# Performance work log

Measured on AMD Instinct MI355X. Metric: run time of the kernel, lower is better.

## Reference

```python
import jax, jax.numpy as jnp
import numpy as np
import math

WINDOW = 1024
B, H, E, D = 4, 8, 64, 64


def setup_inputs() -> dict:
    key = jax.random.key(0)
    kq, kk, kv, ks = jax.random.split(key, 4)
    queries = jax.random.normal(kq, (B, WINDOW, H, E), dtype=jnp.float32)
    keys = jax.random.normal(kk, (B, WINDOW, H, E), dtype=jnp.float32)
    values = jax.random.normal(kv, (B, WINDOW, H, D), dtype=jnp.float32)
    sigma = jax.random.normal(ks, (B, WINDOW, H), dtype=jnp.float32)
    return {"queries": queries, "keys": keys, "values": values, "sigma": sigma}


def reference(queries, keys, values, sigma):
    # queries: [B,L,H,E], keys: [B,S,H,E], values: [B,S,H,D], sigma: [B,L,H]
    Bq, L, Hh, Ee = queries.shape
    scale = 1.0 / math.sqrt(Ee)
    # scores: [B,H,L,S]
    attn = scale * jnp.einsum('blhe,bshe->bhls', queries, keys)
    win = attn.shape[-1]

    # sigma path: [B,L,H] -> [B,H,L]
    sig = jnp.transpose(sigma, (0, 2, 1))
    sig = jax.nn.sigmoid(sig * 5.0) + 1e-5
    sig = jnp.power(3.0, sig) - 1.0          # [B,H,L]
    sig = jnp.broadcast_to(sig[..., None], sig.shape + (win,))  # [B,H,L,S]

    # |i-j| distance matrix [L,S]
    idx = jnp.arange(win, dtype=jnp.float32)
    dist = jnp.abs(idx[:, None] - idx[None, :])

    inv_sqrt_2pi = 1.0 / math.sqrt(2.0 * math.pi)
    prior = inv_sqrt_2pi / sig * jnp.exp(-(dist ** 2) / 2.0 / (sig ** 2))

    series = jax.nn.softmax(attn, axis=-1)   # [B,H,L,S]
    V = jnp.einsum('bhls,bshd->blhd', series, values)
    return V, series, prior, sig
```

## Files before the change

kernel.cpp:

```cpp
#include <hip/hip_runtime.h>
#include <math.h>


typedef __attribute__((ext_vector_type(8))) short short8;
typedef __attribute__((ext_vector_type(4))) float f32x4;

constexpr int Bc = 4, Lc = 1024, Hc = 8, Ec = 64, Dc = 64, Sc = 1024;

constexpr long OFF_V      = 0;
constexpr long OFF_SERIES = (long)Bc * Lc * Hc * Dc;
constexpr long OFF_PRIOR  = OFF_SERIES + (long)Bc * Hc * Lc * Sc;
constexpr long OFF_SIG    = OFF_PRIOR  + (long)Bc * Hc * Lc * Sc;

constexpr long KELEMS = (long)Bc * Lc * Hc * Ec;

#define LOG2E        1.4426950408889634f
#define LOG2_3       1.5849625007211562f
#define INV_SQRT_2PI 0.3989422804014327f
#define HALF_LOG2E   0.7213475204444817f
#define FIVE_LOG2E   7.213475204444817f

__device__ __forceinline__ unsigned short f2bf(float x) {
    unsigned int u = __float_as_uint(x);
    return (unsigned short)((u + 0x7fffu + ((u >> 16) & 1u)) >> 16);
}
__device__ __forceinline__ float bf2f(unsigned short h) {
    return __uint_as_float(((unsigned int)h) << 16);
}
__device__ __forceinline__ void split8(const float* v, short8& hi, short8& lo) {
    #pragma unroll
    for (int j = 0; j < 8; ++j) {
        unsigned short hh = f2bf(v[j]);
        hi[j] = (short)hh;
        lo[j] = (short)f2bf(v[j] - bf2f(hh));
    }
}

__global__ __launch_bounds__(256)
void k_prep(const float* __restrict__ kp, unsigned short* __restrict__ khi,
            unsigned short* __restrict__ klo)
{
    const int i = blockIdx.x * 256 + threadIdx.x;
    const int e4 = i & 15, h = (i >> 4) & 7, s = (i >> 7) & 1023, b = i >> 17;
    const float4 v = reinterpret_cast<const float4*>(kp)[((b * Lc + s) * Hc + h) * 16 + e4];
    const unsigned short h0 = f2bf(v.x), h1 = f2bf(v.y), h2 = f2bf(v.z), h3 = f2bf(v.w);
    uint2 hi, lo;
    hi.x = (unsigned)h0 | ((unsigned)h1 << 16);
    hi.y = (unsigned)h2 | ((unsigned)h3 << 16);
    lo.x = (unsigned)f2bf(v.x - bf2f(h0)) | ((unsigned)f2bf(v.y - bf2f(h1)) << 16);
    lo.y = (unsigned)f2bf(v.z - bf2f(h2)) | ((unsigned)f2bf(v.w - bf2f(h3)) << 16);
    const long dst = ((long)(b * Hc + h) * Lc + s) * 16 + e4;
    reinterpret_cast<uint2*>(khi)[dst] = hi;
    reinterpret_cast<uint2*>(klo)[dst] = lo;
}

__global__ __launch_bounds__(256)
void v_prep(const float* __restrict__ vp, unsigned short* __restrict__ vthi,
            unsigned short* __restrict__ vtlo)
{
    __shared__ float lds[64][68];
    const int blk = blockIdx.x;
    const int bh = blk >> 4, s0 = (blk & 15) * 64;
    const int b = bh >> 3, h = bh & 7;
    const int t = threadIdx.x;
    {
        const int sl = t >> 4, d4 = t & 15;
        #pragma unroll
        for (int r = 0; r < 4; ++r) {
            const int s = sl + r * 16;
            const float4 v = reinterpret_cast<const float4*>(
                vp)[((long)(b * Lc + s0 + s) * Hc + h) * 16 + d4];
            *reinterpret_cast<float4*>(&lds[s][d4 * 4]) = v;
        }
    }
    __syncthreads();
    const int d = t >> 2, a = t & 3;
    #pragma unroll
    for (int jj = 0; jj < 4; ++jj) {
        const int sb = a * 16 + jj * 4;
        const float x0 = lds[sb + 0][d], x1 = lds[sb + 1][d];
        const float x2 = lds[sb + 2][d], x3 = lds[sb + 3][d];
        const unsigned short h0 = f2bf(x0), h1 = f2bf(x1), h2 = f2bf(x2), h3 = f2bf(x3);
        uint2 hi, lo;
        hi.x = (unsigned)h0 | ((unsigned)h1 << 16);
        hi.y = (unsigned)h2 | ((unsigned)h3 << 16);
        lo.x = (unsigned)f2bf(x0 - bf2f(h0)) | ((unsigned)f2bf(x1 - bf2f(h1)) << 16);
        lo.y = (unsigned)f2bf(x2 - bf2f(h2)) | ((unsigned)f2bf(x3 - bf2f(h3)) << 16);
        const long dst = (((long)bh * Dc + d) * Sc + s0 + sb) >> 2;
        reinterpret_cast<uint2*>(vthi)[dst] = hi;
        reinterpret_cast<uint2*>(vtlo)[dst] = lo;
    }
}

__global__ __launch_bounds__(256, 2)
void attn_all(const float* __restrict__ qp,
              const unsigned short* __restrict__ khi,
              const unsigned short* __restrict__ klo,
              const unsigned short* __restrict__ vthi,
              const unsigned short* __restrict__ vtlo,
              const float* __restrict__ sigp, float* __restrict__ out)
{
    __shared__ float Plds[4][4096];

    const int bid = blockIdx.x;
    const int swz = (bid & 7) * 256 + (bid >> 3);
    const int rowblk = swz & 63, bh = swz >> 6;
    const int b = bh >> 3, h = bh & 7;
    const int row0 = rowblk * 16;
    const int t = threadIdx.x;
    const int w = t >> 6;
    const int lane = t & 63;
    const int ln = lane & 15, kg = lane >> 4;
    float* const Pw = Plds[w];

    short8 qhi[2], qlo[2];
    {
        const float* qrow = qp + ((long)(b * Lc + row0 + ln) * Hc + h) * Ec;
        #pragma unroll
        for (int kc = 0; kc < 2; ++kc) {
            const float* qq = qrow + kc * 32 + kg * 8;
            const float4 qa = *reinterpret_cast<const float4*>(qq);
            const float4 qb = *reinterpret_cast<const float4*>(qq + 4);
            float qv[8] = {qa.x, qa.y, qa.z, qa.w, qb.x, qb.y, qb.z, qb.w};
            split8(qv, qhi[kc], qlo[kc]);
        }
    }

    f32x4 p[16];
    const long kcb = (long)bh * Lc;
    #pragma unroll
    for (int tt = 0; tt < 16; ++tt) {
        const int col = w * 256 + tt * 16 + ln;
        const unsigned short* kb = khi + (kcb + col) * Ec + kg * 8;
        const unsigned short* kl = klo + (kcb + col) * Ec + kg * 8;
        const short8 bh0 = *reinterpret_cast<const short8*>(kb);
        const short8 bl0 = *reinterpret_cast<const short8*>(kl);
        const short8 bh1 = *reinterpret_cast<const short8*>(kb + 32);
        const short8 bl1 = *reinterpret_cast<const short8*>(kl + 32);
        f32x4 a = {0.f, 0.f, 0.f, 0.f};
        a = __builtin_amdgcn_mfma_f32_16x16x32_bf16(qhi[0], bh0, a, 0, 0, 0);
        a = __builtin_amdgcn_mfma_f32_16x16x32_bf16(qlo[0], bh0, a, 0, 0, 0);
        a = __builtin_amdgcn_mfma_f32_16x16x32_bf16(qhi[0], bl0, a, 0, 0, 0);
        a = __builtin_amdgcn_mfma_f32_16x16x32_bf16(qhi[1], bh1, a, 0, 0, 0);
        a = __builtin_amdgcn_mfma_f32_16x16x32_bf16(qlo[1], bh1, a, 0, 0, 0);
        a = __builtin_amdgcn_mfma_f32_16x16x32_bf16(qhi[1], bl1, a, 0, 0, 0);
        p[tt] = a;
    }

    const float C = 0.125f * LOG2E;
    float sl4[4] = {0.f, 0.f, 0.f, 0.f};
    #pragma unroll
    for (int tt = 0; tt < 16; ++tt) {
        #pragma unroll
        for (int i = 0; i < 4; ++i) {
            const float e = __builtin_exp2f(p[tt][i] * C);
            p[tt][i] = e; sl4[i] += e;
        }
    }
    #pragma unroll
    for (int off = 1; off < 16; off <<= 1) {
        #pragma unroll
        for (int i = 0; i < 4; ++i) sl4[i] += __shfl_xor(sl4[i], off, 64);
    }
    if (ln == 0) {
        #pragma unroll
        for (int i = 0; i < 4; ++i) Pw[kg * 4 + i] = sl4[i];
    }
    __syncthreads();
    float inv[4];
    #pragma unroll
    for (int i = 0; i < 4; ++i) {
        const int rr = kg * 4 + i;
        inv[i] = 1.0f / (Plds[0][rr] + Plds[1][rr] + Plds[2][rr] + Plds[3][rr]);
    }
    __syncthreads();

    #pragma unroll
    for (int tt = 0; tt < 16; ++tt) {
        #pragma unroll
        for (int i = 0; i < 4; ++i) {
            const float v = p[tt][i] * inv[i];
            Pw[(kg * 4 + i) * 256 + tt * 16 + ln] = v;
        }
    }

    {
        const long sbase = OFF_SERIES + ((long)bh * Lc + row0) * Sc + w * 256;
        #pragma unroll
        for (int r = 0; r < 16; ++r) {
            const float4 v = *reinterpret_cast<const float4*>(&Pw[r * 256 + lane * 4]);
            *reinterpret_cast<float4*>(&out[sbase + (long)r * Sc + lane * 4]) = v;
        }
    }

    f32x4 acc2[4];
    #pragma unroll
    for (int dt = 0; dt < 4; ++dt) acc2[dt] = (f32x4){0.f, 0.f, 0.f, 0.f};
    #pragma unroll
    for (int kc = 0; kc < 8; ++kc) {
        const float* pa = &Pw[ln * 256 + kc * 32 + kg * 8];
        const float4 a0 = *reinterpret_cast<const float4*>(pa);
        const float4 a1 = *reinterpret_cast<const float4*>(pa + 4);
        float av[8] = {a0.x, a0.y, a0.z, a0.w, a1.x, a1.y, a1.z, a1.w};
        short8 phi, plo;
        split8(av, phi, plo);
        #pragma unroll
        for (int dt = 0; dt < 4; ++dt) {
            const long vb = ((long)bh * Dc + dt * 16 + ln) * Sc + w * 256 + kc * 32 + kg * 8;
            const short8 vh = *reinterpret_cast<const short8*>(vthi + vb);
            const short8 vl = *reinterpret_cast<const short8*>(vtlo + vb);
            acc2[dt] = __builtin_amdgcn_mfma_f32_16x16x32_bf16(phi, vh, acc2[dt], 0, 0, 0);
            acc2[dt] = __builtin_amdgcn_mfma_f32_16x16x32_bf16(plo, vh, acc2[dt], 0, 0, 0);
            acc2[dt] = __builtin_amdgcn_mfma_f32_16x16x32_bf16(phi, vl, acc2[dt], 0, 0, 0);
        }
    }

    #pragma unroll
    for (int dt = 0; dt < 4; ++dt) {
        #pragma unroll
        for (int i = 0; i < 4; ++i)
            Pw[(kg * 4 + i) * 68 + dt * 16 + ln] = acc2[dt][i];
    }
    __syncthreads();
    {
        const int r = t >> 4, d0 = (t & 15) * 4;
        const float4 s0 = *reinterpret_cast<const float4*>(&Plds[0][r * 68 + d0]);
        const float4 s1 = *reinterpret_cast<const float4*>(&Plds[1][r * 68 + d0]);
        const float4 s2 = *reinterpret_cast<const float4*>(&Plds[2][r * 68 + d0]);
        const float4 s3 = *reinterpret_cast<const float4*>(&Plds[3][r * 68 + d0]);
        float4 vs;
        vs.x = s0.x + s1.x + s2.x + s3.x;
        vs.y = s0.y + s1.y + s2.y + s3.y;
        vs.z = s0.z + s1.z + s2.z + s3.z;
        vs.w = s0.w + s1.w + s2.w + s3.w;
        *reinterpret_cast<float4*>(
            &out[OFF_V + ((long)(b * Lc + row0 + r) * Hc + h) * Dc + d0]) = vs;
    }

    {
        const int c0 = t * 4;
        #pragma unroll 4
        for (int r = 0; r < 16; ++r) {
            const int lg = row0 + r;
            const float x = sigp[(long)(b * Lc + lg) * Hc + h];
            const float sgm = 1.0f / (1.0f + __builtin_exp2f(-FIVE_LOG2E * x)) + 1e-5f;
            const float sg = __builtin_exp2f(LOG2_3 * sgm) - 1.0f;
            const float amp = INV_SQRT_2PI / sg;
            const float ce = -HALF_LOG2E / (sg * sg);
            const long rowbase = ((long)bh * Lc + lg) * Sc;
            const float df = (float)(c0 - lg);
            float4 pr;
            pr.x = amp * __builtin_exp2f(ce * df * df);
            const float d1 = df + 1.f; pr.y = amp * __builtin_exp2f(ce * d1 * d1);
            const float d2 = df + 2.f; pr.z = amp * __builtin_exp2f(ce * d2 * d2);
            const float d3 = df + 3.f; pr.w = amp * __builtin_exp2f(ce * d3 * d3);
            *reinterpret_cast<float4*>(&out[OFF_PRIOR + rowbase + c0]) = pr;
            *reinterpret_cast<float4*>(&out[OFF_SIG + rowbase + c0]) =
                make_float4(sg, sg, sg, sg);
        }
    }
}

extern "C" void kernel_launch(void* const* d_in, const int* in_sizes, int n_in,
                              void* d_out, int out_size, void* d_ws, size_t ws_size,
                              hipStream_t stream) {
    const float* q  = (const float*)d_in[0];
    const float* k  = (const float*)d_in[1];
    const float* v  = (const float*)d_in[2];
    const float* sg = (const float*)d_in[3];
    float* out = (float*)d_out;

    unsigned short* khi  = (unsigned short*)d_ws;
    unsigned short* klo  = khi + KELEMS;
    unsigned short* vthi = klo + KELEMS;
    unsigned short* vtlo = vthi + KELEMS;

    hipLaunchKernelGGL(k_prep, dim3(2048), dim3(256), 0, stream, k, khi, klo);
    hipLaunchKernelGGL(v_prep, dim3(512), dim3(256), 0, stream, v, vthi, vtlo);
    hipLaunchKernelGGL(attn_all, dim3(2048), dim3(256), 0, stream,
                       q, khi, klo, vthi, vtlo, sg, out);
}
```

Baseline: 571.3 us.

## Fuse exp into QK loop, defer softmax normalization, and pad LDS rows

Computes exp right after each QK MFMA tile and writes the unnormalized probabilities straight to LDS instead of holding all 16 score tiles in registers. Normalization moves to the series store and the final PV accumulator, which removes one barrier and a separate rescale pass. LDS rows are padded to a pitch of 258 to cut bank conflicts, and the PV loop is reordered so each output tile's accumulation runs to completion. The occupancy hint on launch bounds is dropped. The odd pitch leaves some float4 LDS accesses only 8-byte aligned, which may make them slower or split them.

Result: faster. 553.1 us (-3.2%).

```diff
diff --git a/kernel.cpp b/kernel.cpp
--- a/kernel.cpp
+++ b/kernel.cpp
@@ -19,6 +19,8 @@
 #define INV_SQRT_2PI 0.3989422804014327f
 #define HALF_LOG2E   0.7213475204444817f
 #define FIVE_LOG2E   7.213475204444817f
+
+#define PPITCH 258
 
 __device__ __forceinline__ unsigned short f2bf(float x) {
     unsigned int u = __float_as_uint(x);
@@ -92,7 +94,7 @@
     }
 }
 
-__global__ __launch_bounds__(256, 2)
+__global__ __launch_bounds__(256)
 void attn_all(const float* __restrict__ qp,
               const unsigned short* __restrict__ khi,
               const unsigned short* __restrict__ klo,
@@ -100,7 +102,8 @@
               const unsigned short* __restrict__ vtlo,
               const float* __restrict__ sigp, float* __restrict__ out)
 {
-    __shared__ float Plds[4][4096];
+    __shared__ float Pw_all[4][16 * PPITCH];
+    __shared__ float red[4][16];
 
     const int bid = blockIdx.x;
     const int swz = (bid & 7) * 256 + (bid >> 3);
@@ -111,7 +114,7 @@
     const int w = t >> 6;
     const int lane = t & 63;
     const int ln = lane & 15, kg = lane >> 4;
-    float* const Pw = Plds[w];
+    float* const Pw = Pw_all[w];
 
     short8 qhi[2], qlo[2];
     {
@@ -126,7 +129,8 @@
         }
     }
 
-    f32x4 p[16];
+    const float C = 0.125f * LOG2E;
+    float sl4[4] = {0.f, 0.f, 0.f, 0.f};
     const long kcb = (long)bh * Lc;
     #pragma unroll
     for (int tt = 0; tt < 16; ++tt) {
@@ -144,19 +148,14 @@
         a = __builtin_amdgcn_mfma_f32_16x16x32_bf16(qhi[1], bh1, a, 0, 0, 0);
         a = __builtin_amdgcn_mfma_f32_16x16x32_bf16(qlo[1], bh1, a, 0, 0, 0);
         a = __builtin_amdgcn_mfma_f32_16x16x32_bf16(qhi[1], bl1, a, 0, 0, 0);
-        p[tt] = a;
-    }
-
-    const float C = 0.125f * LOG2E;
-    float sl4[4] = {0.f, 0.f, 0.f, 0.f};
-    #pragma unroll
-    for (int tt = 0; tt < 16; ++tt) {
         #pragma unroll
         for (int i = 0; i < 4; ++i) {
-            const float e = __builtin_exp2f(p[tt][i] * C);
-            p[tt][i] = e; sl4[i] += e;
-        }
-    }
+            const float e = __builtin_exp2f(a[i] * C);
+            sl4[i] += e;
+            Pw[(kg * 4 + i) * PPITCH + tt * 16 + ln] = e;
+        }
+    }
+
     #pragma unroll
     for (int off = 1; off < 16; off <<= 1) {
         #pragma unroll
@@ -164,70 +163,61 @@
     }
     if (ln == 0) {
         #pragma unroll
-        for (int i = 0; i < 4; ++i) Pw[kg * 4 + i] = sl4[i];
+        for (int i = 0; i < 4; ++i) red[w][kg * 4 + i] = sl4[i];
     }
     __syncthreads();
-    float inv[4];
+    float inv4[4];
     #pragma unroll
     for (int i = 0; i < 4; ++i) {
         const int rr = kg * 4 + i;
-        inv[i] = 1.0f / (Plds[0][rr] + Plds[1][rr] + Plds[2][rr] + Plds[3][rr]);
-    }
-    __syncthreads();
-
-    #pragma unroll
-    for (int tt = 0; tt < 16; ++tt) {
-        #pragma unroll
-        for (int i = 0; i < 4; ++i) {
-            const float v = p[tt][i] * inv[i];
-            Pw[(kg * 4 + i) * 256 + tt * 16 + ln] = v;
-        }
+        inv4[i] = 1.0f / (red[0][rr] + red[1][rr] + red[2][rr] + red[3][rr]);
     }
 
     {
         const long sbase = OFF_SERIES + ((long)bh * Lc + row0) * Sc + w * 256;
         #pragma unroll
         for (int r = 0; r < 16; ++r) {
-            const float4 v = *reinterpret_cast<const float4*>(&Pw[r * 256 + lane * 4]);
+            const float ivr = 1.0f / (red[0][r] + red[1][r] + red[2][r] + red[3][r]);
+            float4 v = *reinterpret_cast<const float4*>(&Pw[r * PPITCH + lane * 4]);
+            v.x *= ivr; v.y *= ivr; v.z *= ivr; v.w *= ivr;
             *reinterpret_cast<float4*>(&out[sbase + (long)r * Sc + lane * 4]) = v;
         }
     }
 
-    f32x4 acc2[4];
-    #pragma unroll
-    for (int dt = 0; dt < 4; ++dt) acc2[dt] = (f32x4){0.f, 0.f, 0.f, 0.f};
+    short8 pahi[8], palo[8];
     #pragma unroll
     for (int kc = 0; kc < 8; ++kc) {
-        const float* pa = &Pw[ln * 256 + kc * 32 + kg * 8];
+        const float* pa = &Pw[ln * PPITCH + kc * 32 + kg * 8];
         const float4 a0 = *reinterpret_cast<const float4*>(pa);
         const float4 a1 = *reinterpret_cast<const float4*>(pa + 4);
         float av[8] = {a0.x, a0.y, a0.z, a0.w, a1.x, a1.y, a1.z, a1.w};
-        short8 phi, plo;
-        split8(av, phi, plo);
-        #pragma unroll
-        for (int dt = 0; dt < 4; ++dt) {
-            const long vb = ((long)bh * Dc + dt * 16 + ln) * Sc + w * 256 + kc * 32 + kg * 8;
-            const short8 vh = *reinterpret_cast<const short8*>(vthi + vb);
-            const short8 vl = *reinterpret_cast<const short8*>(vtlo + vb);
-            acc2[dt] = __builtin_amdgcn_mfma_f32_16x16x32_bf16(phi, vh, acc2[dt], 0, 0, 0);
-            acc2[dt] = __builtin_amdgcn_mfma_f32_16x16x32_bf16(plo, vh, acc2[dt], 0, 0, 0);
-            acc2[dt] = __builtin_amdgcn_mfma_f32_16x16x32_bf16(phi, vl, acc2[dt], 0, 0, 0);
-        }
+        split8(av, pahi[kc], palo[kc]);
     }
 
     #pragma unroll
     for (int dt = 0; dt < 4; ++dt) {
+        f32x4 acc = {0.f, 0.f, 0.f, 0.f};
+        const long vrow = ((long)bh * Dc + dt * 16 + ln) * Sc + w * 256 + kg * 8;
+        #pragma unroll
+        for (int kc = 0; kc < 8; ++kc) {
+            const short8 vh = *reinterpret_cast<const short8*>(vthi + vrow + kc * 32);
+            const short8 vl = *reinterpret_cast<const short8*>(vtlo + vrow + kc * 32);
+            acc = __builtin_amdgcn_mfma_f32_16x16x32_bf16(pahi[kc], vh, acc, 0, 0, 0);
+            acc = __builtin_amdgcn_mfma_f32_16x16x32_bf16(palo[kc], vh, acc, 0, 0, 0);
+            acc = __builtin_amdgcn_mfma_f32_16x16x32_bf16(pahi[kc], vl, acc, 0, 0, 0);
+        }
         #pragma unroll
         for (int i = 0; i < 4; ++i)
-            Pw[(kg * 4 + i) * 68 + dt * 16 + ln] = acc2[dt][i];
+            Pw[(kg * 4 + i) * 68 + dt * 16 + ln] = acc[i] * inv4[i];
     }
     __syncthreads();
+
     {
         const int r = t >> 4, d0 = (t & 15) * 4;
-        const float4 s0 = *reinterpret_cast<const float4*>(&Plds[0][r * 68 + d0]);
-        const float4 s1 = *reinterpret_cast<const float4*>(&Plds[1][r * 68 + d0]);
-        const float4 s2 = *reinterpret_cast<const float4*>(&Plds[2][r * 68 + d0]);
-        const float4 s3 = *reinterpret_cast<const float4*>(&Plds[3][r * 68 + d0]);
+        const float4 s0 = *reinterpret_cast<const float4*>(&Pw_all[0][r * 68 + d0]);
+        const float4 s1 = *reinterpret_cast<const float4*>(&Pw_all[1][r * 68 + d0]);
+        const float4 s2 = *reinterpret_cast<const float4*>(&Pw_all[2][r * 68 + d0]);
+        const float4 s3 = *reinterpret_cast<const float4*>(&Pw_all[3][r * 68 + d0]);
         float4 vs;
         vs.x = s0.x + s1.x + s2.x + s3.x;
         vs.y = s0.y + s1.y + s2.y + s3.y;
```
